# Optimization experiments

Measured on AMD Instinct MI355X. Metric: run time of the kernel, lower is better.

## Reference

```python
import jax, jax.numpy as jnp
import numpy as np

D_MODEL = 1024
HEAD_SIZE = 64
B, T = 4, 4096


def setup_inputs() -> dict:
    key = jax.random.key(0)
    k1, k2, k3, k4, k5, k6 = jax.random.split(key, 6)
    q = jax.random.normal(k1, (B, T, D_MODEL), dtype=jnp.float32)
    k = jax.random.normal(k2, (B, T, D_MODEL), dtype=jnp.float32)
    v = jax.random.normal(k3, (B, T, D_MODEL), dtype=jnp.float32)
    # bias-free Linear weights stored as [d_model, head_size] so proj = x @ W
    s = 1.0 / np.sqrt(D_MODEL)
    Wq = jax.random.uniform(k4, (D_MODEL, HEAD_SIZE), jnp.float32, -s, s)
    Wk = jax.random.uniform(k5, (D_MODEL, HEAD_SIZE), jnp.float32, -s, s)
    Wv = jax.random.uniform(k6, (D_MODEL, HEAD_SIZE), jnp.float32, -s, s)
    # [T,T] bool mask, True = keep (lower-triangular, exercises masking path)
    attn_mask = jnp.tril(jnp.ones((T, T), dtype=jnp.bool_))
    return {"q": q, "k": k, "v": v, "Wq": Wq, "Wk": Wk, "Wv": Wv,
            "attn_mask": attn_mask}


def reference(q, k, v, Wq, Wk, Wv, attn_mask):
    # projections: [B,T,d_model] @ [d_model,head] -> [B,T,head]
    qh = q @ Wq
    kh = k @ Wk
    vh = v @ Wv
    # raw scores [B,T,T]; attention_operation is Identity
    att = jnp.einsum('bqh,bkh->bqk', qh, kh)
    # mask BEFORE scaling (matches original; -inf/scale == -inf)
    att = jnp.where(attn_mask[None, :, :], att, -jnp.inf)
    scale = jnp.asarray(HEAD_SIZE ** 0.5, att.dtype)
    probs = jax.nn.softmax(att / scale, axis=-1)
    # dropout rate is 0.0 -> no-op
    return jnp.einsum('bqk,bkh->bqh', probs, vh)
```

## Files before the change

### kernel.cpp

```cpp
#include <hip/hip_runtime.h>
#include <hip/hip_fp16.h>

typedef _Float16 f16;
typedef __fp16 h16x2 __attribute__((ext_vector_type(2)));
typedef _Float16 f16x8 __attribute__((ext_vector_type(8)));
typedef _Float16 f16x4v __attribute__((ext_vector_type(4)));
typedef float f32x4 __attribute__((ext_vector_type(4)));
typedef float f32x16 __attribute__((ext_vector_type(16)));
typedef unsigned int u32;
typedef u32 u32x4 __attribute__((ext_vector_type(4)));

constexpr int DM = 1024;
constexpr int HS = 64;
constexpr int NBATCH = 4;
constexpr int T = 4096;
constexpr float CEXP = 0.18033688011112042f;

#if __has_builtin(__builtin_amdgcn_exp2f)
#define EXP2(x) __builtin_amdgcn_exp2f(x)
#else
#define EXP2(x) exp2f(x)
#endif

static __device__ __forceinline__ u32 pack2_f16(float a, float b) {
  union { f16 h[2]; u32 u; } cv;
  cv.h[0] = (f16)a; cv.h[1] = (f16)b;
  return cv.u;
}

static __device__ __forceinline__ f16x8 cvt8(const f32x4& a0, const f32x4& a1) {
  union { h16x2 p[4]; f16x8 v; } cv;
  cv.p[0] = __builtin_amdgcn_cvt_pkrtz(a0[0], a0[1]);
  cv.p[1] = __builtin_amdgcn_cvt_pkrtz(a0[2], a0[3]);
  cv.p[2] = __builtin_amdgcn_cvt_pkrtz(a1[0], a1[1]);
  cv.p[3] = __builtin_amdgcn_cvt_pkrtz(a1[2], a1[3]);
  return cv.v;
}

static __device__ __forceinline__ void gload_lds16(const void* g, void* l) {
  __builtin_amdgcn_global_load_lds(
      (__attribute__((address_space(1))) void*)(g),
      (__attribute__((address_space(3))) void*)(l), 16, 0, 0);
}

__global__ void wtrans_kernel(const float* __restrict__ Wq, const float* __restrict__ Wk,
                              const float* __restrict__ Wv, f16* __restrict__ WTf) {
  const int which = blockIdx.y;
  const float* __restrict__ W = (which == 0) ? Wq : ((which == 1) ? Wk : Wv);
  const int o8 = blockIdx.x * 256 + threadIdx.x;
  const int t = o8 >> 8;
  const int cb = (o8 >> 6) & 3;
  const int g = (o8 >> 4) & 3;
  const int q15 = o8 & 15;
  const int col = cb * 16 + q15;
  f16x8 v;
#pragma unroll
  for (int e = 0; e < 8; ++e) v[e] = (f16)W[(t * 32 + 8 * g + e) * 64 + col];
  *(f16x8*)(WTf + which * 65536 + o8 * 8) = v;
}

__global__ __launch_bounds__(256) void proj_kernel(
    const float* __restrict__ xq, const float* __restrict__ xk, const float* __restrict__ xv,
    const f16* __restrict__ WTf, f16* __restrict__ qh, f16* __restrict__ kh,
    f16* __restrict__ vhT) {
  __shared__ __align__(16) char Bs[131072];

  const int which = blockIdx.y;
  const float* __restrict__ x = (which == 0) ? xq : ((which == 1) ? xk : xv);
  const int tid = threadIdx.x;
  const int lane = tid & 63, w = tid >> 6;
  const int q15 = lane & 15, g = lane >> 4;
  const int row0 = blockIdx.x * 64 + w * 16;

  const char* __restrict__ wsrc = (const char*)(WTf + (size_t)which * 65536);
#pragma unroll
  for (int j = 0; j < 32; ++j)
    gload_lds16(wsrc + j * 4096 + w * 1024 + (lane & 63) * 16,
                &Bs[j * 4096 + w * 1024]);
  __builtin_amdgcn_sched_barrier(0);

  const size_t aaddr =
      (size_t)((const char*)x + (size_t)(row0 + q15) * 4096 + 32 * g);
  f32x4 ld[16][4];
#define AISSUE(s)                                                                       \
  {                                                                                     \
    const size_t ab = aaddr + (size_t)((s) * 256);                                      \
    asm volatile("global_load_dwordx4 %0, %1, off"            : "=v"(ld[s][0]) : "v"(ab)); \
    asm volatile("global_load_dwordx4 %0, %1, off offset:16"  : "=v"(ld[s][1]) : "v"(ab)); \
    asm volatile("global_load_dwordx4 %0, %1, off offset:128" : "=v"(ld[s][2]) : "v"(ab)); \
    asm volatile("global_load_dwordx4 %0, %1, off offset:144" : "=v"(ld[s][3]) : "v"(ab)); \
  }
  AISSUE(0) AISSUE(1) AISSUE(2) AISSUE(3)

  asm volatile("s_waitcnt vmcnt(16)" ::: "memory");
  __builtin_amdgcn_sched_barrier(0);
  __builtin_amdgcn_s_barrier();
  __builtin_amdgcn_sched_barrier(0);

  f32x4 acc[4];
#pragma unroll
  for (int cb = 0; cb < 4; ++cb) acc[cb] = (f32x4){0.f, 0.f, 0.f, 0.f};

#pragma unroll
  for (int s = 0; s < 16; ++s) {
    if (s < 13)      asm volatile("s_waitcnt vmcnt(12)" ::: "memory");
    else if (s == 13) asm volatile("s_waitcnt vmcnt(8)" ::: "memory");
    else if (s == 14) asm volatile("s_waitcnt vmcnt(4)" ::: "memory");
    else              asm volatile("s_waitcnt vmcnt(0)" ::: "memory");
    __builtin_amdgcn_sched_barrier(0);
    if (s + 4 < 16) AISSUE(s + 4)

    const f16x8 af0 = cvt8(ld[s][0], ld[s][1]);
    const f16x8 af1 = cvt8(ld[s][2], ld[s][3]);
    const char* bb = &Bs[0] + s * 8192 + lane * 16;
#pragma unroll
    for (int cb = 0; cb < 4; ++cb) {
      const f16x8 b0 = *(const f16x8*)(bb + cb * 1024);
      acc[cb] = __builtin_amdgcn_mfma_f32_16x16x32_f16(af0, b0, acc[cb], 0, 0, 0);
    }
#pragma unroll
    for (int cb = 0; cb < 4; ++cb) {
      const f16x8 b1 = *(const f16x8*)(bb + 4096 + cb * 1024);
      acc[cb] = __builtin_amdgcn_mfma_f32_16x16x32_f16(af1, b1, acc[cb], 0, 0, 0);
    }
  }
#undef AISSUE

  if (which < 2) {
    f16* __restrict__ outp = (which == 0) ? qh : kh;
#pragma unroll
    for (int cb = 0; cb < 4; ++cb)
#pragma unroll
      for (int j = 0; j < 4; ++j)
        outp[(size_t)(row0 + 4 * g + j) * HS + cb * 16 + q15] = (f16)acc[cb][j];
  } else {
    const int b = row0 >> 12;
    const int t0 = (row0 & (T - 1)) + 4 * g;
#pragma unroll
    for (int cb = 0; cb < 4; ++cb) {
      f16x4v pv;
#pragma unroll
      for (int j = 0; j < 4; ++j) pv[j] = (f16)acc[cb][j];
      *(f16x4v*)(vhT + (size_t)b * HS * T + (size_t)(cb * 16 + q15) * T + t0) = pv;
    }
  }
}

__global__ __launch_bounds__(512, 4) void attn_kernel(
    const f16* __restrict__ qh, const f16* __restrict__ kh,
    const f16* __restrict__ vhT, float* __restrict__ out) {
  __shared__ float sO[4][64][33];
  __shared__ float sMm[8][32];
  __shared__ float sLs[8][32];

  const int tid = threadIdx.x;
  const int lane = tid & 63, w = tid >> 6;
  const int q31 = lane & 31, hi = lane >> 5;

  const int id = blockIdx.x;
  const int b = (id & 7) >> 1;
  const int qt = 127 - 2 * (id >> 3) - (id & 1);
  const int q0 = qt * 32;

  const f16* __restrict__ kbase = kh + (size_t)b * T * HS;
  const f16* __restrict__ vbase = vhT + (size_t)b * HS * T;
  const f16* __restrict__ qp = qh + (size_t)(b * T + q0 + q31) * HS + 8 * hi;

  f16x8 qb[4];
#pragma unroll
  for (int kt = 0; kt < 4; ++kt) qb[kt] = *(const f16x8*)(qp + 16 * kt);

  f32x16 o0, o1;
#pragma unroll
  for (int i = 0; i < 16; ++i) { o0[i] = 0.f; o1[i] = 0.f; }
  float m = -1e30f, lsum = 0.f;

  const int nblk = qt + 1;
  for (int blk = w; blk < nblk; blk += 8) {
    const int kv0 = blk * 32;
    const f16* kr = kbase + (size_t)(kv0 + q31) * HS + 8 * hi;
    f16x8 ka0 = *(const f16x8*)(kr);
    f16x8 ka1 = *(const f16x8*)(kr + 16);
    f16x8 ka2 = *(const f16x8*)(kr + 32);
    f16x8 ka3 = *(const f16x8*)(kr + 48);

    f32x16 s;
#pragma unroll
    for (int i = 0; i < 16; ++i) s[i] = 0.f;
    s = __builtin_amdgcn_mfma_f32_32x32x16_f16(ka0, qb[0], s, 0, 0, 0);
    s = __builtin_amdgcn_mfma_f32_32x32x16_f16(ka1, qb[1], s, 0, 0, 0);
    s = __builtin_amdgcn_mfma_f32_32x32x16_f16(ka2, qb[2], s, 0, 0, 0);
    s = __builtin_amdgcn_mfma_f32_32x32x16_f16(ka3, qb[3], s, 0, 0, 0);

    const f16* vr = vbase + (size_t)q31 * T + kv0 + 8 * hi;
    f16x8 v00 = *(const f16x8*)(vr);
    f16x8 v01 = *(const f16x8*)(vr + 16);
    f16x8 v10 = *(const f16x8*)(vr + (size_t)32 * T);
    f16x8 v11 = *(const f16x8*)(vr + (size_t)32 * T + 16);

    if (blk == qt) {
#pragma unroll
      for (int r = 0; r < 16; ++r) {
        const int kl = (r & 3) + 8 * (r >> 2) + 4 * hi;
        if (kl > q31) s[r] = -1e30f;
      }
    }

    float pm = s[0];
#pragma unroll
    for (int r = 1; r < 16; ++r) pm = fmaxf(pm, s[r]);
    pm = fmaxf(pm, __shfl_xor(pm, 32));
    if (!__all(pm <= m + 32.f)) {
      const float mn = fmaxf(m, pm);
      const float r = EXP2((m - mn) * CEXP);
      lsum *= r;
#pragma unroll
      for (int i = 0; i < 16; ++i) { o0[i] *= r; o1[i] *= r; }
      m = mn;
    }

    float p[16];
    float ps = 0.f;
#pragma unroll
    for (int r = 0; r < 16; ++r) { p[r] = EXP2((s[r] - m) * CEXP); ps += p[r]; }
    ps += __shfl_xor(ps, 32);
    lsum += ps;

    u32 c[8], xg[8];
#pragma unroll
    for (int i = 0; i < 8; ++i) c[i] = pack2_f16(p[2 * i], p[2 * i + 1]);
#pragma unroll
    for (int i = 0; i < 8; ++i) xg[i] = (u32)__shfl_xor((int)c[i], 32);
    union { u32x4 u; f16x8 f; } f1, f2;
    f1.u = (u32x4){ hi ? xg[2] : c[0], hi ? xg[3] : c[1], hi ? c[2] : xg[0], hi ? c[3] : xg[1] };
    f2.u = (u32x4){ hi ? xg[6] : c[4], hi ? xg[7] : c[5], hi ? c[6] : xg[4], hi ? c[7] : xg[5] };

    o0 = __builtin_amdgcn_mfma_f32_32x32x16_f16(v00, f1.f, o0, 0, 0, 0);
    o0 = __builtin_amdgcn_mfma_f32_32x32x16_f16(v01, f2.f, o0, 0, 0, 0);
    o1 = __builtin_amdgcn_mfma_f32_32x32x16_f16(v10, f1.f, o1, 0, 0, 0);
    o1 = __builtin_amdgcn_mfma_f32_32x32x16_f16(v11, f2.f, o1, 0, 0, 0);
  }

  if (lane < 32) sMm[w][q31] = m;
  __syncthreads();
  float M = sMm[0][q31];
#pragma unroll
  for (int w2 = 1; w2 < 8; ++w2) M = fmaxf(M, sMm[w2][q31]);
  const float sc = EXP2((m - M) * CEXP);
  if (lane < 32) sLs[w][q31] = lsum * sc;
#pragma unroll
  for (int i = 0; i < 16; ++i) { o0[i] *= sc; o1[i] *= sc; }

  if (w >= 4) {
#pragma unroll
    for (int r = 0; r < 16; ++r) {
      const int d = (r & 3) + 8 * (r >> 2) + 4 * hi;
      sO[w - 4][d][q31] = o0[r];
      sO[w - 4][d + 32][q31] = o1[r];
    }
  }
  __syncthreads();
  if (w < 4) {
#pragma unroll
    for (int r = 0; r < 16; ++r) {
      const int d = (r & 3) + 8 * (r >> 2) + 4 * hi;
      sO[w][d][q31] += o0[r];
      sO[w][d + 32][q31] += o1[r];
    }
  }
  __syncthreads();

  const int q = tid >> 4;
  const int d0 = (tid & 15) * 4;
  float L = 0.f;
#pragma unroll
  for (int w2 = 0; w2 < 8; ++w2) L += sLs[w2][q];
  const float invL = 1.f / L;
  float4 rv;
  rv.x = (sO[0][d0 + 0][q] + sO[1][d0 + 0][q] + sO[2][d0 + 0][q] + sO[3][d0 + 0][q]) * invL;
  rv.y = (sO[0][d0 + 1][q] + sO[1][d0 + 1][q] + sO[2][d0 + 1][q] + sO[3][d0 + 1][q]) * invL;
  rv.z = (sO[0][d0 + 2][q] + sO[1][d0 + 2][q] + sO[2][d0 + 2][q] + sO[3][d0 + 2][q]) * invL;
  rv.w = (sO[0][d0 + 3][q] + sO[1][d0 + 3][q] + sO[2][d0 + 3][q] + sO[3][d0 + 3][q]) * invL;
  *(float4*)(out + (size_t)(b * T + q0 + q) * HS + d0) = rv;
}

extern "C" void kernel_launch(void* const* d_in, const int* in_sizes, int n_in,
                              void* d_out, int out_size, void* d_ws, size_t ws_size,
                              hipStream_t stream) {
  const float* q  = (const float*)d_in[0];
  const float* k  = (const float*)d_in[1];
  const float* v  = (const float*)d_in[2];
  const float* Wq = (const float*)d_in[3];
  const float* Wk = (const float*)d_in[4];
  const float* Wv = (const float*)d_in[5];
  float* out = (float*)d_out;

  f16* qh  = (f16*)d_ws;
  f16* kh  = qh  + (size_t)NBATCH * T * HS;
  f16* vhT = kh  + (size_t)NBATCH * T * HS;
  f16* WTf = vhT + (size_t)NBATCH * T * HS;

  wtrans_kernel<<<dim3(32, 3), 256, 0, stream>>>(Wq, Wk, Wv, WTf);
  proj_kernel<<<dim3(256, 3), 256, 0, stream>>>(q, k, v, WTf, qh, kh, vhT);
  attn_kernel<<<dim3(T / 32 * NBATCH), 512, 0, stream>>>(qh, kh, vhT, out);
}
```

Before: 91.19 us.

## Process four row tiles per projection block to reuse LDS-staged weights

Each projection block now computes 256 rows instead of 64. It loops over four row tiles while keeping the 128KB transposed weight tile resident in LDS, and uses a rotating 8-slot register buffer for the streamed activation loads. The goal is to cut the repeated global-to-LDS weight staging done by every block. In exchange the grid shrinks from 768 to 192 blocks, which leaves many CUs idle on a 256-CU device. The accumulator register count also grows four times, which may hurt memory-level parallelism on a bandwidth-bound pass.

```diff
diff --git a/kernel.cpp b/kernel.cpp
--- a/kernel.cpp
+++ b/kernel.cpp
@@ -59,7 +59,7 @@
   *(f16x8*)(WTf + which * 65536 + o8 * 8) = v;
 }
 
-__global__ __launch_bounds__(256) void proj_kernel(
+__global__ __launch_bounds__(256, 1) void proj_kernel(
     const float* __restrict__ xq, const float* __restrict__ xk, const float* __restrict__ xv,
     const f16* __restrict__ WTf, f16* __restrict__ qh, f16* __restrict__ kh,
     f16* __restrict__ vhT) {
@@ -70,78 +70,86 @@
   const int tid = threadIdx.x;
   const int lane = tid & 63, w = tid >> 6;
   const int q15 = lane & 15, g = lane >> 4;
-  const int row0 = blockIdx.x * 64 + w * 16;
 
   const char* __restrict__ wsrc = (const char*)(WTf + (size_t)which * 65536);
 #pragma unroll
   for (int j = 0; j < 32; ++j)
-    gload_lds16(wsrc + j * 4096 + w * 1024 + (lane & 63) * 16,
-                &Bs[j * 4096 + w * 1024]);
+    gload_lds16(wsrc + j * 4096 + w * 1024 + lane * 16, &Bs[j * 4096 + w * 1024]);
   __builtin_amdgcn_sched_barrier(0);
 
-  const size_t aaddr =
-      (size_t)((const char*)x + (size_t)(row0 + q15) * 4096 + 32 * g);
-  f32x4 ld[16][4];
-#define AISSUE(s)                                                                       \
-  {                                                                                     \
-    const size_t ab = aaddr + (size_t)((s) * 256);                                      \
-    asm volatile("global_load_dwordx4 %0, %1, off"            : "=v"(ld[s][0]) : "v"(ab)); \
-    asm volatile("global_load_dwordx4 %0, %1, off offset:16"  : "=v"(ld[s][1]) : "v"(ab)); \
-    asm volatile("global_load_dwordx4 %0, %1, off offset:128" : "=v"(ld[s][2]) : "v"(ab)); \
-    asm volatile("global_load_dwordx4 %0, %1, off offset:144" : "=v"(ld[s][3]) : "v"(ab)); \
-  }
-  AISSUE(0) AISSUE(1) AISSUE(2) AISSUE(3)
+  const size_t abase = (size_t)((const char*)x +
+      ((size_t)blockIdx.x * 256 + w * 16 + q15) * 4096 + 32 * g);
+
+#define AISSUE(slot, G2)                                                        \
+  {                                                                             \
+    const size_t ab = abase + (size_t)((G2) >> 4) * 262144           \
+                    + (size_t)((G2) & 15) * 256;                                \
+    asm volatile("global_load_dwordx4 %0, %1, off"            : "=v"(ld[slot][0]) : "v"(ab)); \
+    asm volatile("global_load_dwordx4 %0, %1, off offset:16"  : "=v"(ld[slot][1]) : "v"(ab)); \
+    asm volatile("global_load_dwordx4 %0, %1, off offset:128" : "=v"(ld[slot][2]) : "v"(ab)); \
+    asm volatile("global_load_dwordx4 %0, %1, off offset:144" : "=v"(ld[slot][3]) : "v"(ab)); \
+  }
+
+  f32x4 ld[8][4];
+  AISSUE(0, 0) AISSUE(1, 1) AISSUE(2, 2) AISSUE(3, 3)
 
   asm volatile("s_waitcnt vmcnt(16)" ::: "memory");
   __builtin_amdgcn_sched_barrier(0);
   __builtin_amdgcn_s_barrier();
   __builtin_amdgcn_sched_barrier(0);
 
-  f32x4 acc[4];
-#pragma unroll
-  for (int cb = 0; cb < 4; ++cb) acc[cb] = (f32x4){0.f, 0.f, 0.f, 0.f};
-
-#pragma unroll
-  for (int s = 0; s < 16; ++s) {
-    if (s < 13)      asm volatile("s_waitcnt vmcnt(12)" ::: "memory");
-    else if (s == 13) asm volatile("s_waitcnt vmcnt(8)" ::: "memory");
-    else if (s == 14) asm volatile("s_waitcnt vmcnt(4)" ::: "memory");
+  f32x4 acc[4][4];
+#pragma unroll
+  for (int t = 0; t < 4; ++t)
+#pragma unroll
+    for (int cb = 0; cb < 4; ++cb) acc[t][cb] = (f32x4){0.f, 0.f, 0.f, 0.f};
+
+#pragma unroll
+  for (int G = 0; G < 64; ++G) {
+    const int t = G >> 4, s = G & 15, slot = G & 7;
+    if (G < 61)      asm volatile("s_waitcnt vmcnt(12)" ::: "memory");
+    else if (G == 61) asm volatile("s_waitcnt vmcnt(8)" ::: "memory");
+    else if (G == 62) asm volatile("s_waitcnt vmcnt(4)" ::: "memory");
     else              asm volatile("s_waitcnt vmcnt(0)" ::: "memory");
     __builtin_amdgcn_sched_barrier(0);
-    if (s + 4 < 16) AISSUE(s + 4)
-
-    const f16x8 af0 = cvt8(ld[s][0], ld[s][1]);
-    const f16x8 af1 = cvt8(ld[s][2], ld[s][3]);
+    if (G + 4 < 64) AISSUE((G + 4) & 7, G + 4)
+
+    const f16x8 af0 = cvt8(ld[slot][0], ld[slot][1]);
+    const f16x8 af1 = cvt8(ld[slot][2], ld[slot][3]);
     const char* bb = &Bs[0] + s * 8192 + lane * 16;
 #pragma unroll
     for (int cb = 0; cb < 4; ++cb) {
       const f16x8 b0 = *(const f16x8*)(bb + cb * 1024);
-      acc[cb] = __builtin_amdgcn_mfma_f32_16x16x32_f16(af0, b0, acc[cb], 0, 0, 0);
+      acc[t][cb] = __builtin_amdgcn_mfma_f32_16x16x32_f16(af0, b0, acc[t][cb], 0, 0, 0);
     }
 #pragma unroll
     for (int cb = 0; cb < 4; ++cb) {
       const f16x8 b1 = *(const f16x8*)(bb + 4096 + cb * 1024);
-      acc[cb] = __builtin_amdgcn_mfma_f32_16x16x32_f16(af1, b1, acc[cb], 0, 0, 0);
+      acc[t][cb] = __builtin_amdgcn_mfma_f32_16x16x32_f16(af1, b1, acc[t][cb], 0, 0, 0);
     }
   }
 #undef AISSUE
 
-  if (which < 2) {
-    f16* __restrict__ outp = (which == 0) ? qh : kh;
-#pragma unroll
-    for (int cb = 0; cb < 4; ++cb)
-#pragma unroll
-      for (int j = 0; j < 4; ++j)
-        outp[(size_t)(row0 + 4 * g + j) * HS + cb * 16 + q15] = (f16)acc[cb][j];
-  } else {
-    const int b = row0 >> 12;
-    const int t0 = (row0 & (T - 1)) + 4 * g;
-#pragma unroll
-    for (int cb = 0; cb < 4; ++cb) {
-      f16x4v pv;
-#pragma unroll
-      for (int j = 0; j < 4; ++j) pv[j] = (f16)acc[cb][j];
-      *(f16x4v*)(vhT + (size_t)b * HS * T + (size_t)(cb * 16 + q15) * T + t0) = pv;
+#pragma unroll
+  for (int t = 0; t < 4; ++t) {
+    const int row0 = blockIdx.x * 256 + t * 64 + w * 16;
+    if (which < 2) {
+      f16* __restrict__ outp = (which == 0) ? qh : kh;
+#pragma unroll
+      for (int cb = 0; cb < 4; ++cb)
+#pragma unroll
+        for (int j = 0; j < 4; ++j)
+          outp[(size_t)(row0 + 4 * g + j) * HS + cb * 16 + q15] = (f16)acc[t][cb][j];
+    } else {
+      const int b = row0 >> 12;
+      const int t0 = (row0 & (T - 1)) + 4 * g;
+#pragma unroll
+      for (int cb = 0; cb < 4; ++cb) {
+        f16x4v pv;
+#pragma unroll
+        for (int j = 0; j < 4; ++j) pv[j] = (f16)acc[t][cb][j];
+        *(f16x4v*)(vhT + (size_t)b * HS * T + (size_t)(cb * 16 + q15) * T + t0) = pv;
+      }
     }
   }
 }
@@ -301,6 +309,6 @@
   f16* WTf = vhT + (size_t)NBATCH * T * HS;
 
   wtrans_kernel<<<dim3(32, 3), 256, 0, stream>>>(Wq, Wk, Wv, WTf);
-  proj_kernel<<<dim3(256, 3), 256, 0, stream>>>(q, k, v, WTf, qh, kh, vhT);
+  proj_kernel<<<dim3(64, 3), 256, 0, stream>>>(q, k, v, WTf, qh, kh, vhT);
   attn_kernel<<<dim3(T / 32 * NBATCH), 512, 0, stream>>>(qh, kh, vhT, out);
 }
```

Result: faster. 89.30 us (-2.1%).
